# Performance work log

Measured on AMD Instinct MI355X. Metric: run time of the kernel, lower is better.

The kernel has to match this reference:

```python
import jax, jax.numpy as jnp
import numpy as np

N = 50000        # n nodes (cells)
C = 1024         # common genes
H = 128          # edge_h_dim
HG = 128         # edge_hidden
E = 1600000      # edges (avg degree 32)
LAYERS = 2       # gnn_layers (unset in original __init__; fixed here)
EPS = 1e-8


def setup_inputs() -> dict:
    key = jax.random.key(0)
    ks = jax.random.split(key, 10)
    x_common = jax.random.normal(ks[0], (N, C), dtype=jnp.float32)
    src = jax.random.randint(ks[1], (E,), 0, N, dtype=jnp.int32)
    dst = jax.random.randint(ks[2], (E,), 0, N, dtype=jnp.int32)
    base_w = jax.random.uniform(ks[3], (E,), dtype=jnp.float32)
    # encoder params: Linear(C,H) -> ReLU -> Linear(H,H) -> ReLU
    W1 = jax.random.normal(ks[4], (C, H), dtype=jnp.float32) * 0.02
    b1 = jnp.zeros((H,), dtype=jnp.float32)
    W2 = jax.random.normal(ks[5], (H, H), dtype=jnp.float32) * 0.1
    b2 = jnp.zeros((H,), dtype=jnp.float32)
    # edge gate params: Linear(2H, HG) -> ReLU -> Linear(HG, 1)
    Wg1 = jax.random.normal(ks[6], (2 * H, HG), dtype=jnp.float32) * 0.1
    bg1 = jnp.zeros((HG,), dtype=jnp.float32)
    Wg2 = jax.random.normal(ks[7], (HG, 1), dtype=jnp.float32) * 0.1
    bg2 = jnp.full((1,), 2.0, dtype=jnp.float32)  # original init: bias=2.0
    # node reliability logits
    rho_raw = jax.random.normal(ks[8], (N,), dtype=jnp.float32) * 0.5
    return dict(x_common=x_common, src=src, dst=dst, base_w=base_w,
                W1=W1, b1=b1, W2=W2, b2=b2,
                Wg1=Wg1, bg1=bg1, Wg2=Wg2, bg2=bg2, rho_raw=rho_raw)


def reference(x_common, src, dst, base_w, W1, b1, W2, b2, Wg1, bg1, Wg2, bg2, rho_raw):
    # enc: [N, C] -> [N, H]
    h = jax.nn.relu(jax.nn.relu(x_common @ W1 + b1) @ W2 + b2)
    rho = jax.nn.sigmoid(rho_raw)                 # [N]
    rr = rho[src] * rho[dst]                      # [E] per-edge reliability factor
    for _ in range(LAYERS):
        h_src = h[src]                            # [E, H] gather
        h_dst = h[dst]                            # [E, H] gather
        z = jnp.concatenate([h_src, h_dst], axis=1)               # [E, 2H]
        gate = jax.nn.sigmoid(jax.nn.relu(z @ Wg1 + bg1) @ Wg2 + bg2)[:, 0]  # [E]
        w = base_w * gate * rr                    # [E]
        m = jax.ops.segment_sum(w[:, None] * h_src, dst, num_segments=N)     # [N, H]
        deg = jax.ops.segment_sum(w, dst, num_segments=N)                    # [N]
        h = m / (deg[:, None] + EPS)
    return h
```

## Files before the change

kernel.cpp:

```cpp
#include <hip/hip_runtime.h>
#include <stdint.h>

#define NN 50000
#define CC 1024
#define HH 128
#define EE 1600000
#define EPSV 1e-8f
#define SCAN_BLKS 196

typedef __attribute__((ext_vector_type(8))) short bf16x8;
typedef __attribute__((ext_vector_type(4))) float f32x4;
typedef __attribute__((ext_vector_type(2))) float f32x2;

__device__ __forceinline__ unsigned short f32_to_bf16(float f){
  union { float f; uint32_t u; } cv; cv.f = f;
  uint32_t u = cv.u;
  return (unsigned short)((u + 0x7FFFu + ((u >> 16) & 1u)) >> 16);
}
__device__ __forceinline__ float bf16lo_to_f32(uint32_t w){
  union { uint32_t u; float f; } cv; cv.u = w << 16; return cv.f;
}
__device__ __forceinline__ float bf16hi_to_f32(uint32_t w){
  union { uint32_t u; float f; } cv; cv.u = w & 0xFFFF0000u; return cv.f;
}

#define DPP_ADD(x, ctrl) ((x) + __int_as_float(__builtin_amdgcn_update_dpp(0, __float_as_int(x), (ctrl), 0xF, 0xF, true)))

#define GLOAD_LDS16(g, l) __builtin_amdgcn_global_load_lds( \
    (const __attribute__((address_space(1))) uint32_t*)(g), \
    (__attribute__((address_space(3))) uint32_t*)(l), 16, 0, 0)


__global__ __launch_bounds__(256) void k_prep_all(
    const float* __restrict__ W1, const float* __restrict__ W2,
    const float* __restrict__ Wg1,
    unsigned short* __restrict__ W1T, unsigned short* __restrict__ W2T,
    unsigned short* __restrict__ Wg1T){
  int idx = blockIdx.x*256 + threadIdx.x;
  if(idx < 131072){
    int n = idx >> 10, k = idx & 1023;
    W1T[idx] = f32_to_bf16(W1[k*128 + n]);
  } else if(idx < 131072 + 16384){
    int i = idx - 131072;
    int n = i >> 7, k = i & 127;
    W2T[i] = f32_to_bf16(W2[k*128 + n]);
  } else if(idx < 131072 + 16384 + 32768){
    int i = idx - 131072 - 16384;
    int c = i >> 7, k = i & 127;
    int row = (c < 128) ? k : (128 + k);
    int col = (c < 128) ? c : (c - 128);
    Wg1T[i] = f32_to_bf16(Wg1[row*128 + col]);
  }
}


__global__ __launch_bounds__(256) void k_hist(const int* __restrict__ dst,
                                              int* __restrict__ counts,
                                              int* __restrict__ rank){
  int e = blockIdx.x*256 + threadIdx.x;
  if(e < EE) rank[e] = atomicAdd(&counts[dst[e]], 1);
}

__global__ __launch_bounds__(256) void k_scan1(const int* __restrict__ counts,
    int* __restrict__ lexcl, int* __restrict__ bsum){
  __shared__ int buf[256];
  const int t = threadIdx.x, i = blockIdx.x*256 + t;
  int v = (i < NN) ? counts[i] : 0;
  buf[t] = v;
  __syncthreads();
  for(int off = 1; off < 256; off <<= 1){
    int add = (t >= off) ? buf[t-off] : 0;
    __syncthreads();
    buf[t] += add;
    __syncthreads();
  }
  if(i < NN) lexcl[i] = buf[t] - v;
  if(t == 255) bsum[blockIdx.x] = buf[255];
}

__global__ __launch_bounds__(256) void k_scan2(const int* __restrict__ bsum,
    int* __restrict__ bexcl, int* __restrict__ row_ptr){
  __shared__ int buf[256];
  const int t = threadIdx.x;
  int v = (t < SCAN_BLKS) ? bsum[t] : 0;
  buf[t] = v;
  __syncthreads();
  for(int off = 1; off < 256; off <<= 1){
    int add = (t >= off) ? buf[t-off] : 0;
    __syncthreads();
    buf[t] += add;
    __syncthreads();
  }
  if(t < SCAN_BLKS) bexcl[t] = buf[t] - v;
  if(t == 255) row_ptr[NN] = buf[255];
}

__global__ __launch_bounds__(256) void k_scan3(const int* __restrict__ lexcl,
    const int* __restrict__ bexcl, int* __restrict__ row_ptr){
  const int i = blockIdx.x*256 + threadIdx.x;
  if(i >= NN) return;
  row_ptr[i] = lexcl[i] + bexcl[blockIdx.x];
}

__global__ __launch_bounds__(256) void k_fill(const int* __restrict__ src,
    const int* __restrict__ dst, const float* __restrict__ base_w,
    const float* __restrict__ rho_raw, const int* __restrict__ row_ptr,
    const int* __restrict__ rank, float2* __restrict__ scp){
  int e = blockIdx.x*256 + threadIdx.x;
  if(e >= EE) return;
  int s = src[e], d = dst[e];
  int p = row_ptr[d] + rank[e];
  float rs = 1.f/(1.f + __expf(-rho_raw[s]));
  float rd = 1.f/(1.f + __expf(-rho_raw[d]));
  scp[p] = make_float2(base_w[e]*rs*rd, __int_as_float(s));
}


__global__ __launch_bounds__(256) void k_enc1(
    const float* __restrict__ X, const unsigned short* __restrict__ W1T,
    const float* __restrict__ b1, unsigned short* __restrict__ h1)
{
  __shared__ __attribute__((aligned(16))) float          Af[3][32*32];
  __shared__ __attribute__((aligned(16))) unsigned short Bf[3][128*32];

  const int t = threadIdx.x, w = t >> 6, lane = t & 63;
  const int rowL = lane & 15, kq = lane >> 4;
  const int wm = w >> 1, wn = w & 1;
  const int row0 = blockIdx.x * 32;

  const int a_rl = w*8 + (lane >> 3);
  const int a_cl = lane & 7;
  int agr = row0 + a_rl; if(agr >= NN) agr = NN-1;
  const float* a_src = X + (size_t)agr*1024 + (a_cl ^ (a_rl & 7))*4;
  const int b_rl0 = w*32 + (lane >> 2);
  const int b_cl  = lane & 3;
  const int bkey0 = (b_rl0 ^ (b_rl0 >> 2)) & 3;
  const int bkey1 = ((b_rl0+16) ^ ((b_rl0+16) >> 2)) & 3;
  const unsigned short* b_src0 = W1T + (size_t)b_rl0*1024 + (b_cl ^ bkey0)*8;
  const unsigned short* b_src1 = W1T + (size_t)(b_rl0+16)*1024 + (b_cl ^ bkey1)*8;

  #define STAGE(buf, k0)  do{                                              \
    GLOAD_LDS16(a_src  + (k0), &Af[buf][(w*8)*32]);                        \
    GLOAD_LDS16(b_src0 + (k0), &Bf[buf][(w*32     )*32]);                  \
    GLOAD_LDS16(b_src1 + (k0), &Bf[buf][(w*32 + 16)*32]);                  \
  }while(0)

  f32x4 acc[4] = {};
  const int arow  = wm*16 + rowL;
  const int akey  = rowL & 7;
  const int bkeyR = (rowL ^ (rowL >> 2)) & 3;

  auto COMPUTE = [&](const float* afb, const unsigned short* bfb){
    f32x4 x0 = *(const f32x4*)&afb[arow*32 + (((2*kq  ) ^ akey) << 2)];
    f32x4 x1 = *(const f32x4*)&afb[arow*32 + (((2*kq+1) ^ akey) << 2)];
    union { bf16x8 v; unsigned short s[8]; } pk;
    #pragma unroll
    for(int j = 0; j < 4; j++){ pk.s[j] = f32_to_bf16(x0[j]); pk.s[4+j] = f32_to_bf16(x1[j]); }
    bf16x8 bfr[4];
    #pragma unroll
    for(int nf = 0; nf < 4; nf++){
      const int br = wn*64 + nf*16 + rowL;
      bfr[nf] = *(const bf16x8*)&bfb[br*32 + ((kq ^ bkeyR) << 3)];
    }
    #pragma unroll
    for(int nf = 0; nf < 4; nf++)
      acc[nf] = __builtin_amdgcn_mfma_f32_16x16x32_bf16(pk.v, bfr[nf], acc[nf], 0, 0, 0);
  };

  #define STEP(cbuf, sbuf, sk, vN)  do{                                    \
    if((sk) >= 0) STAGE(sbuf, (sk)*32);                                    \
    asm volatile("s_waitcnt vmcnt(" #vN ")" ::: "memory");                 \
    __builtin_amdgcn_s_barrier();                                          \
    __builtin_amdgcn_sched_barrier(0);                                     \
    COMPUTE(&Af[cbuf][0], &Bf[cbuf][0]);                                   \
    __builtin_amdgcn_s_barrier();                                          \
  }while(0)

  STAGE(0, 0);
  STAGE(1, 32);

  for(int tt = 0; tt < 30; tt += 3){
    STEP(0, 2, tt + 2, 6);
    STEP(1, 0, tt + 3, 6);
    STEP(2, 1, tt + 4, 6);
  }
  STEP(0, 0, -1, 3);
  asm volatile("s_waitcnt vmcnt(0)" ::: "memory");
  __builtin_amdgcn_s_barrier();
  __builtin_amdgcn_sched_barrier(0);
  COMPUTE(&Af[1][0], &Bf[1][0]);
  #undef STEP
  #undef STAGE

  #pragma unroll
  for(int nf = 0; nf < 4; nf++){
    const int col = wn*64 + nf*16 + rowL;
    const float bv = b1[col];
    #pragma unroll
    for(int r = 0; r < 4; r++){
      const int gr = row0 + wm*16 + kq*4 + r;
      if(gr < NN) h1[(size_t)gr*128 + col] = f32_to_bf16(fmaxf(acc[nf][r] + bv, 0.f));
    }
  }
}


__device__ __forceinline__ void uv_phase2(
    const unsigned short* hs, const unsigned short* wgl, int row0, int wave, int lane,
    const float* __restrict__ bg1,
    unsigned short* __restrict__ UH, float* __restrict__ Vf)
{
  const int rowL = lane & 15, kq = lane >> 4;
  const int r = wave*16 + rowL;
  f32x4 acc[16] = {};
  #pragma unroll
  for(int ks = 0; ks < 4; ks++){
    const int kc = ks*4 + kq;
    bf16x8 a = *(const bf16x8*)&hs[r*128 + ((kc ^ (r & 15)) << 3)];
    #pragma unroll
    for(int nt = 0; nt < 16; nt++){
      bf16x8 b = *(const bf16x8*)&wgl[(nt*16 + rowL)*128 + ((kc ^ rowL) << 3)];
      acc[nt] = __builtin_amdgcn_mfma_f32_16x16x32_bf16(a, b, acc[nt], 0, 0, 0);
    }
  }
  #pragma unroll
  for(int nt = 0; nt < 16; nt++){
    const int col = nt*16 + rowL;
    #pragma unroll
    for(int rr = 0; rr < 4; rr++){
      const int gr = row0 + wave*16 + kq*4 + rr;
      if(gr < NN){
        if(col < 128) UH[(size_t)gr*256 + col] = f32_to_bf16(acc[nt][rr]);
        else          Vf[(size_t)gr*128 + col - 128] = acc[nt][rr] + bg1[col - 128];
      }
    }
  }
}


__global__ __launch_bounds__(256) void k_uvA(
    const unsigned short* __restrict__ h1, const unsigned short* __restrict__ W2T,
    const float* __restrict__ b2, const unsigned short* __restrict__ Wg1T,
    const float* __restrict__ bg1, unsigned short* __restrict__ UH,
    float* __restrict__ Vf)
{
  __shared__ __attribute__((aligned(16))) unsigned short hs[64*128];
  __shared__ __attribute__((aligned(16))) unsigned short wgl[256*128];
  const int t = threadIdx.x, wave = t >> 6, lane = t & 63;
  const int rowL = lane & 15, kq = lane >> 4;
  const int row0 = blockIdx.x*64;

  bf16x8 wreg[16];
  #pragma unroll
  for(int i = 0; i < 16; i++)
    wreg[i] = *(const bf16x8*)(Wg1T + (i*256 + t)*8);

  int ar = row0 + wave*16 + rowL; if(ar >= NN) ar = NN-1;
  f32x4 acc[8] = {};
  #pragma unroll
  for(int ks = 0; ks < 4; ks++){
    bf16x8 a = *(const bf16x8*)(h1 + (size_t)ar*128 + ks*32 + kq*8);
    #pragma unroll
    for(int nt = 0; nt < 8; nt++){
      bf16x8 b = *(const bf16x8*)(W2T + (nt*16 + rowL)*128 + ks*32 + kq*8);
      acc[nt] = __builtin_amdgcn_mfma_f32_16x16x32_bf16(a, b, acc[nt], 0, 0, 0);
    }
  }
  #pragma unroll
  for(int nt = 0; nt < 8; nt++){
    const int col = nt*16 + rowL;
    const float bv = b2[col];
    #pragma unroll
    for(int r = 0; r < 4; r++){
      const int rw = wave*16 + kq*4 + r;
      const unsigned short hv = f32_to_bf16(fmaxf(acc[nt][r] + bv, 0.f));
      hs[rw*128 + (((col >> 3) ^ (rw & 15)) << 3) + (col & 7)] = hv;
    }
  }
  #pragma unroll
  for(int i = 0; i < 16; i++){
    const int idx = i*256 + t, row = idx >> 4, c = idx & 15;
    *(bf16x8*)&wgl[row*128 + ((c ^ (row & 15)) << 3)] = wreg[i];
  }
  __syncthreads();
  {
    const int r = t >> 2, gr = row0 + r;
    if(gr < NN){
      #pragma unroll
      for(int j8 = 0; j8 < 4; j8++){
        const int chunk = (t & 3)*4 + j8;
        bf16x8 v = *(const bf16x8*)&hs[r*128 + ((chunk ^ (r & 15)) << 3)];
        *(bf16x8*)&UH[(size_t)gr*256 + 128 + chunk*8] = v;
      }
    }
  }
  uv_phase2(hs, wgl, row0, wave, lane, bg1, UH, Vf);
}


__global__ __launch_bounds__(256) void k_uvB(
    const float* __restrict__ hf, const unsigned short* __restrict__ Wg1T,
    const float* __restrict__ bg1, unsigned short* __restrict__ UH,
    float* __restrict__ Vf)
{
  __shared__ __attribute__((aligned(16))) unsigned short hs[64*128];
  __shared__ __attribute__((aligned(16))) unsigned short wgl[256*128];
  const int t = threadIdx.x, wave = t >> 6, lane = t & 63;
  const int row0 = blockIdx.x*64;

  bf16x8 wreg[16];
  #pragma unroll
  for(int i = 0; i < 16; i++)
    wreg[i] = *(const bf16x8*)(Wg1T + (i*256 + t)*8);

  {
    const int r = t >> 2, gr0 = row0 + r;
    const int gr = (gr0 < NN) ? gr0 : NN-1;
    const float* p = hf + (size_t)gr*128 + (t & 3)*32;
    #pragma unroll
    for(int j8 = 0; j8 < 4; j8++){
      f32x4 v0 = *(const f32x4*)(p + j8*8);
      f32x4 v1 = *(const f32x4*)(p + j8*8 + 4);
      union { bf16x8 v; unsigned short s[8]; } pk;
      #pragma unroll
      for(int j = 0; j < 4; j++){ pk.s[j] = f32_to_bf16(v0[j]); pk.s[4+j] = f32_to_bf16(v1[j]); }
      const int chunk = (t & 3)*4 + j8;
      *(bf16x8*)&hs[r*128 + ((chunk ^ (r & 15)) << 3)] = pk.v;
      if(gr0 < NN) *(bf16x8*)&UH[(size_t)gr0*256 + 128 + chunk*8] = pk.v;
    }
  }
  #pragma unroll
  for(int i = 0; i < 16; i++){
    const int idx = i*256 + t, row = idx >> 4, c = idx & 15;
    *(bf16x8*)&wgl[row*128 + ((c ^ (row & 15)) << 3)] = wreg[i];
  }
  __syncthreads();
  uv_phase2(hs, wgl, row0, wave, lane & 63, bg1, UH, Vf);
}


__global__ __launch_bounds__(256) void k_gate_agg(
    const unsigned short* __restrict__ UH, const float* __restrict__ Vf,
    const int* __restrict__ row_ptr, const float2* __restrict__ scp,
    const float* __restrict__ Wg2, const float* __restrict__ bg2p,
    float* __restrict__ out_f32)
{
  __shared__ float2 ws_s[4][64];
  const int wv = threadIdx.x >> 6, lane = threadIdx.x & 63;
  const int gw = blockIdx.x*4 + wv;
  if(gw >= NN) return;
  const int eq = lane >> 4, li = lane & 15;

  f32x4 va = *(const f32x4*)(Vf + (size_t)gw*128 + li*8);
  f32x4 vb = *(const f32x4*)(Vf + (size_t)gw*128 + li*8 + 4);
  f32x4 wa = *(const f32x4*)(Wg2 + li*8);
  f32x4 wb = *(const f32x4*)(Wg2 + li*8 + 4);
  const float vch[8]  = {va[0],va[1],va[2],va[3],vb[0],vb[1],vb[2],vb[3]};
  const float w2ch[8] = {wa[0],wa[1],wa[2],wa[3],wb[0],wb[1],wb[2],wb[3]};
  const float bg2v = bg2p[0];

  const int beg = row_ptr[gw], end = row_ptr[gw+1];
  float a0 = 0.f, a1 = 0.f, wsum = 0.f;

  for(int base = beg; base < end; base += 64){
    const int nb = min(64, end - base);

    float2 sc_c0, sc_c1; bf16x8 u_c0, u_c1;
    {
      const int i0 = (eq     < nb) ? eq     : 0;
      const int i1 = (4 + eq < nb) ? 4 + eq : 0;
      sc_c0 = scp[base + i0]; sc_c1 = scp[base + i1];
      u_c0 = *(const bf16x8*)&UH[(uint32_t)__float_as_int(sc_c0.y)*256u + li*8];
      u_c1 = *(const bf16x8*)&UH[(uint32_t)__float_as_int(sc_c1.y)*256u + li*8];
    }
    for(int q = 0; q < nb; q += 8){
      float2 sc_n0 = sc_c0, sc_n1 = sc_c1; bf16x8 u_n0 = u_c0, u_n1 = u_c1;
      if(q + 8 < nb){
        const int i0 = (q + 8  + eq < nb) ? q + 8  + eq : 0;
        const int i1 = (q + 12 + eq < nb) ? q + 12 + eq : 0;
        sc_n0 = scp[base + i0]; sc_n1 = scp[base + i1];
        u_n0 = *(const bf16x8*)&UH[(uint32_t)__float_as_int(sc_n0.y)*256u + li*8];
        u_n1 = *(const bf16x8*)&UH[(uint32_t)__float_as_int(sc_n1.y)*256u + li*8];
      }
      {
        union { bf16x8 v; uint32_t u32[4]; } uu; uu.v = u_c0;
        float tacc = 0.f;
        #pragma unroll
        for(int p = 0; p < 4; p++){
          const uint32_t w2b = uu.u32[p];
          tacc += fmaxf(bf16lo_to_f32(w2b) + vch[2*p],   0.f) * w2ch[2*p];
          tacc += fmaxf(bf16hi_to_f32(w2b) + vch[2*p+1], 0.f) * w2ch[2*p+1];
        }
        tacc = DPP_ADD(tacc, 0xB1);
        tacc = DPP_ADD(tacc, 0x4E);
        tacc = DPP_ADD(tacc, 0x141);
        tacc = DPP_ADD(tacc, 0x140);
        const float g = 1.f/(1.f + __expf(-(tacc + bg2v)));
        const int idx = q + eq;
        if(li == 0 && idx < nb) ws_s[wv][idx] = make_float2(sc_c0.x*g, sc_c0.y);
      }
      {
        union { bf16x8 v; uint32_t u32[4]; } uu; uu.v = u_c1;
        float tacc = 0.f;
        #pragma unroll
        for(int p = 0; p < 4; p++){
          const uint32_t w2b = uu.u32[p];
          tacc += fmaxf(bf16lo_to_f32(w2b) + vch[2*p],   0.f) * w2ch[2*p];
          tacc += fmaxf(bf16hi_to_f32(w2b) + vch[2*p+1], 0.f) * w2ch[2*p+1];
        }
        tacc = DPP_ADD(tacc, 0xB1);
        tacc = DPP_ADD(tacc, 0x4E);
        tacc = DPP_ADD(tacc, 0x141);
        tacc = DPP_ADD(tacc, 0x140);
        const float g = 1.f/(1.f + __expf(-(tacc + bg2v)));
        const int idx = q + 4 + eq;
        if(li == 0 && idx < nb) ws_s[wv][idx] = make_float2(sc_c1.x*g, sc_c1.y);
      }
      sc_c0 = sc_n0; sc_c1 = sc_n1; u_c0 = u_n0; u_c1 = u_n1;
    }

    #pragma unroll 8
    for(int j = 0; j < nb; j++){
      const float2 p = ws_s[wv][j];
      const float w  = p.x;
      const uint32_t s = (uint32_t)__float_as_int(p.y);
      const uint32_t hw = *(const uint32_t*)&UH[s*256u + 128u + lane*2];
      a0 += w*bf16lo_to_f32(hw);
      a1 += w*bf16hi_to_f32(hw);
      wsum += w;
    }
  }
  const float inv = 1.f/(wsum + EPSV);
  const size_t o = (size_t)gw*128 + lane*2;
  *(f32x2*)&out_f32[o] = (f32x2){a0*inv, a1*inv};
}


extern "C" void kernel_launch(void* const* d_in, const int* in_sizes, int n_in,
                              void* d_out, int out_size, void* d_ws, size_t ws_size,
                              hipStream_t stream) {
  (void)in_sizes; (void)n_in; (void)out_size; (void)ws_size;
  const float* X      = (const float*)d_in[0];
  const int*   src    = (const int*)d_in[1];
  const int*   dst    = (const int*)d_in[2];
  const float* base_w = (const float*)d_in[3];
  const float* W1     = (const float*)d_in[4];
  const float* b1     = (const float*)d_in[5];
  const float* W2     = (const float*)d_in[6];
  const float* b2     = (const float*)d_in[7];
  const float* Wg1    = (const float*)d_in[8];
  const float* bg1    = (const float*)d_in[9];
  const float* Wg2    = (const float*)d_in[10];
  const float* bg2    = (const float*)d_in[11];
  const float* rho    = (const float*)d_in[12];

  char* ws = (char*)d_ws;
  size_t off = 0;
  auto alloc = [&](size_t bytes)->char*{ char* p = ws + off; off += (bytes + 255) & ~(size_t)255; return p; };
  unsigned short* W1T      = (unsigned short*)alloc((size_t)1024*128*2);
  unsigned short* W2T      = (unsigned short*)alloc((size_t)128*128*2);
  unsigned short* Wg1T     = (unsigned short*)alloc((size_t)256*128*2);
  int*            rank     = (int*)alloc((size_t)EE*4);
  float2*         scp      = (float2*)alloc((size_t)EE*8);
  int*            row_ptr  = (int*)alloc((size_t)(NN+1)*4);
  int*            counts   = (int*)alloc((size_t)NN*4);
  int*            lexcl    = (int*)alloc((size_t)NN*4);
  int*            bsum     = (int*)alloc((size_t)256*4);
  int*            bexcl    = (int*)alloc((size_t)256*4);
  unsigned short* h1       = (unsigned short*)alloc((size_t)NN*128*2);
  unsigned short* UH       = (unsigned short*)alloc((size_t)NN*256*2);
  float*          Vf       = (float*)alloc((size_t)NN*128*4);
  float*          hf_B     = (float*)alloc((size_t)NN*128*4);

  hipMemsetAsync(counts, 0, (size_t)NN*4, stream);
  k_prep_all<<<704, 256, 0, stream>>>(W1, W2, Wg1, W1T, W2T, Wg1T);
  k_hist<<<EE/256, 256, 0, stream>>>(dst, counts, rank);
  k_scan1<<<SCAN_BLKS, 256, 0, stream>>>(counts, lexcl, bsum);
  k_scan2<<<1, 256, 0, stream>>>(bsum, bexcl, row_ptr);
  k_scan3<<<SCAN_BLKS, 256, 0, stream>>>(lexcl, bexcl, row_ptr);
  k_fill<<<EE/256, 256, 0, stream>>>(src, dst, base_w, rho, row_ptr, rank, scp);

  k_enc1<<<1563, 256, 0, stream>>>(X, W1T, b1, h1);

  k_uvA<<<782, 256, 0, stream>>>(h1, W2T, b2, Wg1T, bg1, UH, Vf);
  k_gate_agg<<<12500, 256, 0, stream>>>(UH, Vf, row_ptr, scp, Wg2, bg2, hf_B);
  k_uvB<<<782, 256, 0, stream>>>(hf_B, Wg1T, bg1, UH, Vf);
  k_gate_agg<<<12500, 256, 0, stream>>>(UH, Vf, row_ptr, scp, Wg2, bg2, (float*)d_out);
}
```

Baseline: 511.3 us.

## Sub-bucket CSR edges by source stripe to improve gather locality

Edges are now bucketed by (dst, src/6250) into 8 stripes per destination, so each node's edge list is ordered by source region. The histogram, scan and fill kernels are extended to 400k buckets, with a looping single-block mid-level scan. The aim is better cache locality for the random UH row gathers in the gate/aggregate kernels. In exchange, preprocessing gets more expensive with a larger counter array and scan.

After: 510.0 us. No clear change (-0.2%).

```diff
diff --git a/kernel.cpp b/kernel.cpp
--- a/kernel.cpp
+++ b/kernel.cpp
@@ -6,7 +6,10 @@
 #define HH 128
 #define EE 1600000
 #define EPSV 1e-8f
-#define SCAN_BLKS 196
+#define NSTRIPE 8
+#define STRIPE_N 6250
+#define NBUCK (NN*NSTRIPE)
+#define SCAN_BLKS 1563
 
 typedef __attribute__((ext_vector_type(8))) short bf16x8;
 typedef __attribute__((ext_vector_type(4))) float f32x4;
@@ -54,18 +57,20 @@
 }
 
 
-__global__ __launch_bounds__(256) void k_hist(const int* __restrict__ dst,
-                                              int* __restrict__ counts,
-                                              int* __restrict__ rank){
+__global__ __launch_bounds__(256) void k_hist(const int* __restrict__ src,
+    const int* __restrict__ dst, int* __restrict__ counts,
+    int* __restrict__ rank){
   int e = blockIdx.x*256 + threadIdx.x;
-  if(e < EE) rank[e] = atomicAdd(&counts[dst[e]], 1);
+  if(e >= EE) return;
+  int key = dst[e]*NSTRIPE + (int)((unsigned)src[e] / STRIPE_N);
+  rank[e] = atomicAdd(&counts[key], 1);
 }
 
 __global__ __launch_bounds__(256) void k_scan1(const int* __restrict__ counts,
     int* __restrict__ lexcl, int* __restrict__ bsum){
   __shared__ int buf[256];
   const int t = threadIdx.x, i = blockIdx.x*256 + t;
-  int v = (i < NN) ? counts[i] : 0;
+  int v = (i < NBUCK) ? counts[i] : 0;
   buf[t] = v;
   __syncthreads();
   for(int off = 1; off < 256; off <<= 1){
@@ -74,42 +79,51 @@
     buf[t] += add;
     __syncthreads();
   }
-  if(i < NN) lexcl[i] = buf[t] - v;
+  if(i < NBUCK) lexcl[i] = buf[t] - v;
   if(t == 255) bsum[blockIdx.x] = buf[255];
 }
 
-__global__ __launch_bounds__(256) void k_scan2(const int* __restrict__ bsum,
-    int* __restrict__ bexcl, int* __restrict__ row_ptr){
-  __shared__ int buf[256];
+__global__ __launch_bounds__(1024) void k_scan_mid(const int* __restrict__ bsum,
+    int* __restrict__ bexcl){
+  __shared__ int buf[1024];
+  __shared__ int carry_s;
   const int t = threadIdx.x;
-  int v = (t < SCAN_BLKS) ? bsum[t] : 0;
-  buf[t] = v;
+  if(t == 0) carry_s = 0;
   __syncthreads();
-  for(int off = 1; off < 256; off <<= 1){
-    int add = (t >= off) ? buf[t-off] : 0;
+  for(int base = 0; base < SCAN_BLKS; base += 1024){
+    int v = (base+t < SCAN_BLKS) ? bsum[base+t] : 0;
+    buf[t] = v;
     __syncthreads();
-    buf[t] += add;
+    for(int off = 1; off < 1024; off <<= 1){
+      int add = (t >= off) ? buf[t-off] : 0;
+      __syncthreads();
+      buf[t] += add;
+      __syncthreads();
+    }
+    int carry = carry_s;
+    if(base+t < SCAN_BLKS) bexcl[base+t] = carry + buf[t] - v;
     __syncthreads();
-  }
-  if(t < SCAN_BLKS) bexcl[t] = buf[t] - v;
-  if(t == 255) row_ptr[NN] = buf[255];
+    if(t == 1023) carry_s = carry + buf[1023];
+    __syncthreads();
+  }
 }
 
 __global__ __launch_bounds__(256) void k_scan3(const int* __restrict__ lexcl,
-    const int* __restrict__ bexcl, int* __restrict__ row_ptr){
+    const int* __restrict__ bexcl, int* __restrict__ bptr){
   const int i = blockIdx.x*256 + threadIdx.x;
-  if(i >= NN) return;
-  row_ptr[i] = lexcl[i] + bexcl[blockIdx.x];
+  if(i < NBUCK) bptr[i] = lexcl[i] + bexcl[blockIdx.x];
+  if(i == 0) bptr[NBUCK] = EE;
 }
 
 __global__ __launch_bounds__(256) void k_fill(const int* __restrict__ src,
     const int* __restrict__ dst, const float* __restrict__ base_w,
-    const float* __restrict__ rho_raw, const int* __restrict__ row_ptr,
+    const float* __restrict__ rho_raw, const int* __restrict__ bptr,
     const int* __restrict__ rank, float2* __restrict__ scp){
   int e = blockIdx.x*256 + threadIdx.x;
   if(e >= EE) return;
   int s = src[e], d = dst[e];
-  int p = row_ptr[d] + rank[e];
+  int key = d*NSTRIPE + (int)((unsigned)s / STRIPE_N);
+  int p = bptr[key] + rank[e];
   float rs = 1.f/(1.f + __expf(-rho_raw[s]));
   float rd = 1.f/(1.f + __expf(-rho_raw[d]));
   scp[p] = make_float2(base_w[e]*rs*rd, __int_as_float(s));
@@ -341,7 +355,7 @@
 
 __global__ __launch_bounds__(256) void k_gate_agg(
     const unsigned short* __restrict__ UH, const float* __restrict__ Vf,
-    const int* __restrict__ row_ptr, const float2* __restrict__ scp,
+    const int* __restrict__ bptr, const float2* __restrict__ scp,
     const float* __restrict__ Wg2, const float* __restrict__ bg2p,
     float* __restrict__ out_f32)
 {
@@ -359,7 +373,7 @@
   const float w2ch[8] = {wa[0],wa[1],wa[2],wa[3],wb[0],wb[1],wb[2],wb[3]};
   const float bg2v = bg2p[0];
 
-  const int beg = row_ptr[gw], end = row_ptr[gw+1];
+  const int beg = bptr[gw*NSTRIPE], end = bptr[gw*NSTRIPE + NSTRIPE];
   float a0 = 0.f, a1 = 0.f, wsum = 0.f;
 
   for(int base = beg; base < end; base += 64){
@@ -462,28 +476,28 @@
   unsigned short* Wg1T     = (unsigned short*)alloc((size_t)256*128*2);
   int*            rank     = (int*)alloc((size_t)EE*4);
   float2*         scp      = (float2*)alloc((size_t)EE*8);
-  int*            row_ptr  = (int*)alloc((size_t)(NN+1)*4);
-  int*            counts   = (int*)alloc((size_t)NN*4);
-  int*            lexcl    = (int*)alloc((size_t)NN*4);
-  int*            bsum     = (int*)alloc((size_t)256*4);
-  int*            bexcl    = (int*)alloc((size_t)256*4);
+  int*            bptr     = (int*)alloc((size_t)(NBUCK+1)*4);
+  int*            counts   = (int*)alloc((size_t)NBUCK*4);
+  int*            lexcl    = (int*)alloc((size_t)NBUCK*4);
+  int*            bsum     = (int*)alloc((size_t)SCAN_BLKS*4);
+  int*            bexcl    = (int*)alloc((size_t)SCAN_BLKS*4);
   unsigned short* h1       = (unsigned short*)alloc((size_t)NN*128*2);
   unsigned short* UH       = (unsigned short*)alloc((size_t)NN*256*2);
   float*          Vf       = (float*)alloc((size_t)NN*128*4);
   float*          hf_B     = (float*)alloc((size_t)NN*128*4);
 
-  hipMemsetAsync(counts, 0, (size_t)NN*4, stream);
+  hipMemsetAsync(counts, 0, (size_t)NBUCK*4, stream);
   k_prep_all<<<704, 256, 0, stream>>>(W1, W2, Wg1, W1T, W2T, Wg1T);
-  k_hist<<<EE/256, 256, 0, stream>>>(dst, counts, rank);
+  k_hist<<<EE/256, 256, 0, stream>>>(src, dst, counts, rank);
   k_scan1<<<SCAN_BLKS, 256, 0, stream>>>(counts, lexcl, bsum);
-  k_scan2<<<1, 256, 0, stream>>>(bsum, bexcl, row_ptr);
-  k_scan3<<<SCAN_BLKS, 256, 0, stream>>>(lexcl, bexcl, row_ptr);
-  k_fill<<<EE/256, 256, 0, stream>>>(src, dst, base_w, rho, row_ptr, rank, scp);
+  k_scan_mid<<<1, 1024, 0, stream>>>(bsum, bexcl);
+  k_scan3<<<SCAN_BLKS, 256, 0, stream>>>(lexcl, bexcl, bptr);
+  k_fill<<<EE/256, 256, 0, stream>>>(src, dst, base_w, rho, bptr, rank, scp);
 
   k_enc1<<<1563, 256, 0, stream>>>(X, W1T, b1, h1);
 
   k_uvA<<<782, 256, 0, stream>>>(h1, W2T, b2, Wg1T, bg1, UH, Vf);
-  k_gate_agg<<<12500, 256, 0, stream>>>(UH, Vf, row_ptr, scp, Wg2, bg2, hf_B);
+  k_gate_agg<<<12500, 256, 0, stream>>>(UH, Vf, bptr, scp, Wg2, bg2, hf_B);
   k_uvB<<<782, 256, 0, stream>>>(hf_B, Wg1T, bg1, UH, Vf);
-  k_gate_agg<<<12500, 256, 0, stream>>>(UH, Vf, row_ptr, scp, Wg2, bg2, (float*)d_out);
-}
+  k_gate_agg<<<12500, 256, 0, stream>>>(UH, Vf, bptr, scp, Wg2, bg2, (float*)d_out);
+}
```
